# Performance work log

Hardware: AMD Instinct MI355X
Metric: run time of the kernel (lower is better)

The kernel has to match this reference:

```python
import jax, jax.numpy as jnp
import numpy as np

EPS_LN = 1e-6
EPS_NORM = 1e-12


def _l2_normalize(x):
    # F.normalize(p=2, dim=-1): x / max(||x||, eps)
    n = jnp.sqrt(jnp.sum(x * x, axis=-1, keepdims=True))
    return x / jnp.maximum(n, EPS_NORM)


def _layer_norm(x, g, b):
    mu = jnp.mean(x, axis=-1, keepdims=True)
    var = jnp.mean((x - mu) ** 2, axis=-1, keepdims=True)
    return (x - mu) / jnp.sqrt(var + EPS_LN) * g + b


def setup_inputs() -> dict:
    key = jax.random.key(0)
    ks = jax.random.split(key, 4)
    B, S1, S2, H = 16, 2048, 2048, 512
    return {
        "text1_output": jax.random.normal(ks[0], (B, S1, H), dtype=jnp.float32),
        "text2_output": jax.random.normal(ks[1], (B, S2, H), dtype=jnp.float32),
        "text1_mask": jnp.ones((B, S1), dtype=jnp.int32),
        "text2_mask": jnp.ones((B, S2), dtype=jnp.int32),
        "W1": jax.random.normal(ks[2], (H, 2 * H), dtype=jnp.float32) * (1.0 / np.sqrt(H)),
        "b1": jnp.zeros((2 * H,), dtype=jnp.float32),
        "W2": jax.random.normal(ks[3], (2 * H, H), dtype=jnp.float32) * (1.0 / np.sqrt(2 * H)),
        "b2": jnp.zeros((H,), dtype=jnp.float32),
        "ln1_g": jnp.ones((H,), dtype=jnp.float32),
        "ln1_b": jnp.zeros((H,), dtype=jnp.float32),
        "ln2_g": jnp.ones((H,), dtype=jnp.float32),
        "ln2_b": jnp.zeros((H,), dtype=jnp.float32),
    }


def reference(text1_output, text2_output, text1_mask, text2_mask,
              W1, b1, W2, b2, ln1_g, ln1_b, ln2_g, ln2_b):
    # Cosine-similarity cross-attention (dropout = identity, eval mode)
    q_norm = _l2_normalize(text1_output)            # [B,S1,H]
    k_norm = _l2_normalize(text2_output)            # [B,S2,H]
    sim = jnp.einsum('bsh,bth->bst', q_norm, k_norm)  # [B,S1,S2]
    sim = jnp.where(text2_mask[:, None, :] == 0, -jnp.inf, sim)
    attn = jax.nn.softmax(sim, axis=-1)
    out = jnp.einsum('bst,bth->bsh', attn, text2_output)  # [B,S1,H]

    norm_attn = _layer_norm(out, ln1_g, ln1_b)
    resid = norm_attn + text1_output

    ff = jnp.maximum(norm_attn @ W1 + b1, 0.0) @ W2 + b2
    norm_ff = _layer_norm(ff, ln2_g, ln2_b)
    return norm_ff + resid
```

## Files before the change

### kernel.cpp

```cpp
#include <hip/hip_runtime.h>
#include <stdint.h>

#define B_ 16
#define S1_ 2048
#define S2_ 2048
#define H_ 512

typedef short short8 __attribute__((ext_vector_type(8)));
typedef float f32x4 __attribute__((ext_vector_type(4)));

__device__ __forceinline__ unsigned short f2bf(float f) {
  unsigned u = __builtin_bit_cast(unsigned, f);
  u += 0x7fffu + ((u >> 16) & 1u);
  return (unsigned short)(u >> 16);
}
__device__ __forceinline__ float bf2f(unsigned short us) {
  return __builtin_bit_cast(float, (unsigned)us << 16);
}

__device__ __forceinline__ void gload_lds16(const void* g, void* l) {
  __builtin_amdgcn_global_load_lds((const __attribute__((address_space(1))) void*)g,
                                   (__attribute__((address_space(3))) void*)l,
                                   16, 0, 0);
}

__global__ __launch_bounds__(256) void k_cast(const float* __restrict__ x,
                                              unsigned short* __restrict__ y,
                                              float* __restrict__ rn) {
  int row = blockIdx.x * 4 + (threadIdx.x >> 6);
  int l = threadIdx.x & 63;
  const f32x4* xr = (const f32x4*)(x + (size_t)row * H_) + l * 2;
  f32x4 a = xr[0], b = xr[1];
  float s = a[0]*a[0] + a[1]*a[1] + a[2]*a[2] + a[3]*a[3]
          + b[0]*b[0] + b[1]*b[1] + b[2]*b[2] + b[3]*b[3];
#pragma unroll
  for (int m = 1; m < 64; m <<= 1) s += __shfl_xor(s, m);
  if (l == 0) rn[row] = 1.0f / fmaxf(sqrtf(s), 1e-12f);
  short8 o;
#pragma unroll
  for (int i = 0; i < 4; ++i) { o[i] = (short)f2bf(a[i]); o[4 + i] = (short)f2bf(b[i]); }
  *(short8*)(y + (size_t)row * H_ + l * 8) = o;
}

__global__ __launch_bounds__(256) void k_tw(const float* __restrict__ Wm,
                                            unsigned short* __restrict__ WT,
                                            int lgR, int C) {
  int i = blockIdx.x * 256 + threadIdx.x;
  int R = 1 << lgR;
  int n = i >> lgR, k = i & (R - 1);
  WT[i] = f2bf(Wm[(size_t)k * C + n]);
}

__global__ __launch_bounds__(256) void k_tvt(const unsigned short* __restrict__ kn,
                                             unsigned short* __restrict__ vt) {
  __shared__ unsigned short tile[64][72];
  int h0 = blockIdx.x * 64, s0 = blockIdx.y * 64, b = blockIdx.z;
  int t = threadIdx.x;
#pragma unroll
  for (int p = 0; p < 2; ++p) {
    int si = p * 32 + (t >> 3);
    int cj = (t & 7) * 8;
    short8 v = *(const short8*)(kn + ((size_t)(b * S2_ + s0 + si)) * H_ + h0 + cj);
#pragma unroll
    for (int x = 0; x < 8; ++x) tile[si][cj + x] = (unsigned short)v[x];
  }
  __syncthreads();
#pragma unroll
  for (int p = 0; p < 2; ++p) {
    int ho = p * 32 + (t >> 3);
    int sx = (t & 7) * 8;
    short8 o;
#pragma unroll
    for (int x = 0; x < 8; ++x) o[x] = (short)tile[sx + x][ho];
    *(short8*)(vt + ((size_t)(b * H_ + h0 + ho)) * S2_ + s0 + sx) = o;
  }
}

template <int MODE, int SWZ>
__global__ __launch_bounds__(256, 2) void k_gemm(
    const unsigned short* __restrict__ A, const unsigned short* __restrict__ BT,
    const float* __restrict__ bias, const int* __restrict__ mask,
    const float* __restrict__ rq, const float* __restrict__ rk,
    float* __restrict__ lbuf, void* __restrict__ out,
    int M, int N, int K, long sA, long sB, long sOut) {
  __shared__ unsigned short lA[128 * 64];
  __shared__ unsigned short lB[128 * 64];

  int bx, by, z;
  if (SWZ) {
    const int gx = gridDim.x, gy = gridDim.y;
    const int nwg = gx * gy * (int)gridDim.z;
    int orig = ((int)blockIdx.z * gy + (int)blockIdx.y) * gx + (int)blockIdx.x;
    int swzid = ((nwg & 7) == 0) ? ((orig & 7) * (nwg >> 3) + (orig >> 3)) : orig;
    z = swzid / (gx * gy);
    int rem = swzid - z * (gx * gy);
    by = rem / gx;
    bx = rem - by * gx;
  } else {
    bx = blockIdx.x; by = blockIdx.y; z = blockIdx.z;
  }

  const unsigned short* Ab = A + (size_t)z * sA;
  const unsigned short* BTb = BT + (size_t)z * sB;
  const int w = threadIdx.x >> 6, l = threadIdx.x & 63;
  const int lr = l & 15, lk = l >> 4;
  const int m0 = by * 128, n0 = bx * 128;
  const int wm = (w >> 1) * 64, wn = (w & 1) * 64;

  const int srow = l >> 3;
  const int lswz = ((l & 7) * 16) ^ ((srow & 7) << 4);
  const char* pA = (const char*)Ab + ((size_t)(m0 + w * 8 + srow) * K) * 2 + lswz;
  const char* pB = (const char*)BTb + ((size_t)(n0 + w * 8 + srow) * K) * 2 + lswz;
  const size_t rstep = (size_t)K * 64;

  f32x4 acc[4][4];
#pragma unroll
  for (int i = 0; i < 4; ++i)
#pragma unroll
    for (int j = 0; j < 4; ++j) acc[i][j] = (f32x4){0.f, 0.f, 0.f, 0.f};

  const int NT = K >> 6;

#pragma unroll 1
  for (int t = 0; t < NT; ++t) {
    const size_t kb = (size_t)t * 128;
#pragma unroll
    for (int j = 0; j < 4; ++j) {
      gload_lds16(pA + j * rstep + kb, (char*)lA + (j * 4 + w) * 1024);
      gload_lds16(pB + j * rstep + kb, (char*)lB + (j * 4 + w) * 1024);
    }
    asm volatile("s_waitcnt vmcnt(0)" ::: "memory");
    __syncthreads();
#pragma unroll
    for (int s = 0; s < 2; ++s) {
      short8 af[4], bf[4];
#pragma unroll
      for (int mi = 0; mi < 4; ++mi) {
        int row = wm + mi * 16 + lr;
        af[mi] = *(const short8*)(lA + row * 64 + ((s * 32 + lk * 8) ^ ((row & 7) << 3)));
      }
#pragma unroll
      for (int ni = 0; ni < 4; ++ni) {
        int row = wn + ni * 16 + lr;
        bf[ni] = *(const short8*)(lB + row * 64 + ((s * 32 + lk * 8) ^ ((row & 7) << 3)));
      }
#pragma unroll
      for (int mi = 0; mi < 4; ++mi)
#pragma unroll
        for (int ni = 0; ni < 4; ++ni)
          acc[mi][ni] = __builtin_amdgcn_mfma_f32_16x16x32_bf16(af[mi], bf[ni], acc[mi][ni], 0, 0, 0);
    }
    __syncthreads();
  }

  if (MODE == 2) {
    float rqv[4][4], rkv[4], mv[4];
#pragma unroll
    for (int mi = 0; mi < 4; ++mi)
#pragma unroll
      for (int r = 0; r < 4; ++r)
        rqv[mi][r] = rq[(size_t)z * M + m0 + wm + mi * 16 + lk * 4 + r];
#pragma unroll
    for (int ni = 0; ni < 4; ++ni) {
      int gn = n0 + wn + ni * 16 + lr;
      rkv[ni] = rk[(size_t)z * N + gn];
      mv[ni] = (mask[(size_t)z * N + gn] != 0) ? 1.0f : 0.0f;
    }
    float rs[4][4];
#pragma unroll
    for (int mi = 0; mi < 4; ++mi)
#pragma unroll
      for (int r = 0; r < 4; ++r) rs[mi][r] = 0.f;
#pragma unroll
    for (int mi = 0; mi < 4; ++mi)
#pragma unroll
      for (int ni = 0; ni < 4; ++ni) {
        int gn = n0 + wn + ni * 16 + lr;
#pragma unroll
        for (int r = 0; r < 4; ++r) {
          int gm = m0 + wm + mi * 16 + lk * 4 + r;
          float p = __expf(acc[mi][ni][r] * rqv[mi][r] * rkv[ni] - 1.0f) * mv[ni];
          rs[mi][r] += p;
          ((unsigned short*)out)[(size_t)z * sOut + (size_t)gm * N + gn] = f2bf(p);
        }
      }
#pragma unroll
    for (int mi = 0; mi < 4; ++mi)
#pragma unroll
      for (int r = 0; r < 4; ++r) {
        float s = rs[mi][r];
        s += __shfl_xor(s, 1); s += __shfl_xor(s, 2); s += __shfl_xor(s, 4); s += __shfl_xor(s, 8);
        if (lr == 0) {
          int gm = m0 + wm + mi * 16 + lk * 4 + r;
          atomicAdd(&lbuf[(size_t)z * M + gm], s);
        }
      }
  } else if (MODE == 3) {
#pragma unroll
    for (int mi = 0; mi < 4; ++mi)
#pragma unroll
      for (int r = 0; r < 4; ++r) {
        int gm = m0 + wm + mi * 16 + lk * 4 + r;
        float rl = 1.0f / lbuf[(size_t)z * M + gm];
#pragma unroll
        for (int ni = 0; ni < 4; ++ni) {
          int gn = n0 + wn + ni * 16 + lr;
          ((unsigned short*)out)[(size_t)z * sOut + (size_t)gm * N + gn] = f2bf(acc[mi][ni][r] * rl);
        }
      }
  } else {
#pragma unroll
    for (int mi = 0; mi < 4; ++mi)
#pragma unroll
      for (int ni = 0; ni < 4; ++ni) {
        int gn = n0 + wn + ni * 16 + lr;
        float bs = bias[gn];
#pragma unroll
        for (int r = 0; r < 4; ++r) {
          int gm = m0 + wm + mi * 16 + lk * 4 + r;
          float v = acc[mi][ni][r] + bs;
          if (MODE == 0) v = fmaxf(v, 0.f);
          ((unsigned short*)out)[(size_t)gm * N + gn] = f2bf(v);
        }
      }
  }
}

__global__ __launch_bounds__(256) void k_ln1(const unsigned short* __restrict__ O,
                                             const float* __restrict__ g,
                                             const float* __restrict__ bvec,
                                             unsigned short* __restrict__ nattn) {
  int row = blockIdx.x * 4 + (threadIdx.x >> 6);
  int l = threadIdx.x & 63;
  size_t base = (size_t)row * H_ + l * 8;
  short8 ov = *(const short8*)(O + base);
  float x[8];
#pragma unroll
  for (int i = 0; i < 8; ++i) x[i] = bf2f((unsigned short)ov[i]);
  float s = 0.f, q = 0.f;
#pragma unroll
  for (int i = 0; i < 8; ++i) { s += x[i]; q += x[i] * x[i]; }
#pragma unroll
  for (int m = 1; m < 64; m <<= 1) { s += __shfl_xor(s, m); q += __shfl_xor(q, m); }
  float mean = s * (1.f / 512.f);
  float var = q * (1.f / 512.f) - mean * mean;
  float rstd = rsqrtf(var + 1e-6f);
  f32x4 g0 = *(const f32x4*)(g + l * 8), g1v = *(const f32x4*)(g + l * 8 + 4);
  f32x4 b0 = *(const f32x4*)(bvec + l * 8), b1v = *(const f32x4*)(bvec + l * 8 + 4);
  short8 no;
#pragma unroll
  for (int i = 0; i < 4; ++i) {
    no[i]     = (short)f2bf((x[i] - mean) * rstd * g0[i] + b0[i]);
    no[4 + i] = (short)f2bf((x[4 + i] - mean) * rstd * g1v[i] + b1v[i]);
  }
  *(short8*)(nattn + base) = no;
}

__global__ __launch_bounds__(256) void k_ln2(const unsigned short* __restrict__ ff,
                                             const unsigned short* __restrict__ nattn,
                                             const float* __restrict__ text1,
                                             const float* __restrict__ g2,
                                             const float* __restrict__ bb2,
                                             float* __restrict__ out) {
  int row = blockIdx.x * 4 + (threadIdx.x >> 6);
  int l = threadIdx.x & 63;
  size_t base = (size_t)row * H_ + l * 8;
  short8 fv = *(const short8*)(ff + base);
  float x[8];
#pragma unroll
  for (int i = 0; i < 8; ++i) x[i] = bf2f((unsigned short)fv[i]);
  float s = 0.f, q = 0.f;
#pragma unroll
  for (int i = 0; i < 8; ++i) { s += x[i]; q += x[i] * x[i]; }
#pragma unroll
  for (int m = 1; m < 64; m <<= 1) { s += __shfl_xor(s, m); q += __shfl_xor(q, m); }
  float mean = s * (1.f / 512.f);
  float var = q * (1.f / 512.f) - mean * mean;
  float rstd = rsqrtf(var + 1e-6f);
  f32x4 g0 = *(const f32x4*)(g2 + l * 8), g1v = *(const f32x4*)(g2 + l * 8 + 4);
  f32x4 b0 = *(const f32x4*)(bb2 + l * 8), b1v = *(const f32x4*)(bb2 + l * 8 + 4);
  short8 nv = *(const short8*)(nattn + base);
  f32x4 t0 = *(const f32x4*)(text1 + base), t1 = *(const f32x4*)(text1 + base + 4);
  f32x4 o0, o1;
#pragma unroll
  for (int i = 0; i < 4; ++i) {
    o0[i] = (x[i] - mean) * rstd * g0[i] + b0[i] + bf2f((unsigned short)nv[i]) + t0[i];
    o1[i] = (x[4 + i] - mean) * rstd * g1v[i] + b1v[i] + bf2f((unsigned short)nv[4 + i]) + t1[i];
  }
  *(f32x4*)(out + base) = o0;
  *(f32x4*)(out + base + 4) = o1;
}

extern "C" void kernel_launch(void* const* d_in, const int* in_sizes, int n_in,
                              void* d_out, int out_size, void* d_ws, size_t ws_size,
                              hipStream_t stream) {
  const float* text1 = (const float*)d_in[0];
  const float* text2 = (const float*)d_in[1];
  const int* mask2 = (const int*)d_in[3];
  const float* W1 = (const float*)d_in[4];
  const float* b1 = (const float*)d_in[5];
  const float* W2 = (const float*)d_in[6];
  const float* b2 = (const float*)d_in[7];
  const float* g1 = (const float*)d_in[8];
  const float* bb1 = (const float*)d_in[9];
  const float* g2 = (const float*)d_in[10];
  const float* bb2 = (const float*)d_in[11];

  const size_t MiB = 1024ull * 1024ull;
  char* ws = (char*)d_ws;
  unsigned short* W1T   = (unsigned short*)(ws + 0 * MiB);
  unsigned short* W2T   = (unsigned short*)(ws + 1 * MiB);
  float*          lbuf  = (float*)(ws + 2 * MiB);
  float*          rq    = (float*)(ws + 2 * MiB + 256 * 1024);
  float*          rk    = (float*)(ws + 2 * MiB + 512 * 1024);
  unsigned short* qn    = (unsigned short*)(ws + 4 * MiB);
  unsigned short* kn    = (unsigned short*)(ws + 36 * MiB);
  unsigned short* vt    = (unsigned short*)(ws + 68 * MiB);
  unsigned short* P     = (unsigned short*)(ws + 100 * MiB);
  unsigned short* O     = (unsigned short*)(ws + 164 * MiB);
  unsigned short* nattn = (unsigned short*)(ws + 100 * MiB);
  unsigned short* hbuf  = (unsigned short*)(ws + 132 * MiB);
  unsigned short* ffb   = (unsigned short*)(ws + 4 * MiB);
  float* outp = (float*)d_out;

  hipMemsetAsync(lbuf, 0, (size_t)B_ * S1_ * sizeof(float), stream);

  k_cast<<<dim3(B_ * S1_ / 4), 256, 0, stream>>>(text1, qn, rq);
  k_cast<<<dim3(B_ * S2_ / 4), 256, 0, stream>>>(text2, kn, rk);
  k_tw<<<dim3(512 * 1024 / 256), 256, 0, stream>>>(W1, W1T, 9, 1024);
  k_tw<<<dim3(512 * 1024 / 256), 256, 0, stream>>>(W2, W2T, 10, 512);
  k_tvt<<<dim3(H_ / 64, S2_ / 64, B_), 256, 0, stream>>>(kn, vt);

  for (int c = 0; c < 2; ++c) {
    const int c0 = c * 8;
    k_gemm<2, 0><<<dim3(S2_ / 128, S1_ / 128, 8), 256, 0, stream>>>(
        qn + (size_t)c0 * S1_ * H_, kn + (size_t)c0 * S2_ * H_,
        nullptr, mask2 + (size_t)c0 * S2_, rq + (size_t)c0 * S1_, rk + (size_t)c0 * S2_,
        lbuf + (size_t)c0 * S1_, P,
        S1_, S2_, H_, (long)S1_ * H_, (long)S2_ * H_, (long)S1_ * S2_);
    k_gemm<3, 1><<<dim3(H_ / 128, S1_ / 128, 8), 256, 0, stream>>>(
        P, vt + (size_t)c0 * H_ * S2_,
        nullptr, nullptr, nullptr, nullptr,
        lbuf + (size_t)c0 * S1_, O + (size_t)c0 * S1_ * H_,
        S1_, H_, S2_, (long)S1_ * S2_, (long)H_ * S2_, (long)S1_ * H_);
  }

  k_ln1<<<dim3(B_ * S1_ / 4), 256, 0, stream>>>(O, g1, bb1, nattn);
  k_gemm<0, 1><<<dim3(1024 / 128, 32768 / 128, 1), 256, 0, stream>>>(
      nattn, W1T, b1, nullptr, nullptr, nullptr, nullptr, hbuf, 32768, 1024, 512, 0, 0, 0);
  k_gemm<1, 1><<<dim3(512 / 128, 32768 / 128, 1), 256, 0, stream>>>(
      hbuf, W2T, b2, nullptr, nullptr, nullptr, nullptr, ffb, 32768, 512, 1024, 0, 0, 0);
  k_ln2<<<dim3(32768 / 4), 256, 0, stream>>>(ffb, nattn, text1, g2, bb2, outp);
}
```

Baseline: 350.6 us.

## Use FP8 QK similarity GEMM and drop softmax normalization absorbed by LayerNorm

Casts the query and key activations to FP8 e4m3 in the cast kernels and runs the similarity GEMM with FP8 MFMA. Each LDS tile now covers twice the K depth, so global and LDS traffic for that GEMM is halved. It also removes the softmax row-sum accumulation (atomics, memset, and the 1/l scaling in the PV GEMM). This relies on LayerNorm being invariant to a positive per-row scale. The risks are FP8 quantization error in the similarity scores, and a small deviation through the LayerNorm epsilon and bf16 storage of the unnormalized output.

```diff
diff --git a/kernel.cpp b/kernel.cpp
--- a/kernel.cpp
+++ b/kernel.cpp
@@ -24,8 +24,10 @@
                                    16, 0, 0);
 }
 
+template <int WB16>
 __global__ __launch_bounds__(256) void k_cast(const float* __restrict__ x,
                                               unsigned short* __restrict__ y,
+                                              unsigned char* __restrict__ y8,
                                               float* __restrict__ rn) {
   int row = blockIdx.x * 4 + (threadIdx.x >> 6);
   int l = threadIdx.x & 63;
@@ -36,10 +38,18 @@
 #pragma unroll
   for (int m = 1; m < 64; m <<= 1) s += __shfl_xor(s, m);
   if (l == 0) rn[row] = 1.0f / fmaxf(sqrtf(s), 1e-12f);
-  short8 o;
-#pragma unroll
-  for (int i = 0; i < 4; ++i) { o[i] = (short)f2bf(a[i]); o[4 + i] = (short)f2bf(b[i]); }
-  *(short8*)(y + (size_t)row * H_ + l * 8) = o;
+  if (WB16) {
+    short8 o;
+#pragma unroll
+    for (int i = 0; i < 4; ++i) { o[i] = (short)f2bf(a[i]); o[4 + i] = (short)f2bf(b[i]); }
+    *(short8*)(y + (size_t)row * H_ + l * 8) = o;
+  }
+  int p0 = __builtin_amdgcn_cvt_pk_fp8_f32(a[0], a[1], 0, false);
+  p0 = __builtin_amdgcn_cvt_pk_fp8_f32(a[2], a[3], p0, true);
+  int p1 = __builtin_amdgcn_cvt_pk_fp8_f32(b[0], b[1], 0, false);
+  p1 = __builtin_amdgcn_cvt_pk_fp8_f32(b[2], b[3], p1, true);
+  int2 pk = {p0, p1};
+  *(int2*)(y8 + (size_t)row * H_ + l * 8) = pk;
 }
 
 __global__ __launch_bounds__(256) void k_tw(const float* __restrict__ Wm,
@@ -76,15 +86,15 @@
   }
 }
 
-template <int MODE, int SWZ>
+template <int MODE, int SWZ, int FP8>
 __global__ __launch_bounds__(256, 2) void k_gemm(
-    const unsigned short* __restrict__ A, const unsigned short* __restrict__ BT,
+    const void* __restrict__ A, const void* __restrict__ BT,
     const float* __restrict__ bias, const int* __restrict__ mask,
     const float* __restrict__ rq, const float* __restrict__ rk,
-    float* __restrict__ lbuf, void* __restrict__ out,
-    int M, int N, int K, long sA, long sB, long sOut) {
-  __shared__ unsigned short lA[128 * 64];
-  __shared__ unsigned short lB[128 * 64];
+    void* __restrict__ out,
+    int M, int N, int K, long sAbytes, long sBbytes, long sOut) {
+  __shared__ char lA[16384];
+  __shared__ char lB[16384];
 
   int bx, by, z;
   if (SWZ) {
@@ -100,18 +110,17 @@
     bx = blockIdx.x; by = blockIdx.y; z = blockIdx.z;
   }
 
-  const unsigned short* Ab = A + (size_t)z * sA;
-  const unsigned short* BTb = BT + (size_t)z * sB;
   const int w = threadIdx.x >> 6, l = threadIdx.x & 63;
   const int lr = l & 15, lk = l >> 4;
   const int m0 = by * 128, n0 = bx * 128;
   const int wm = (w >> 1) * 64, wn = (w & 1) * 64;
 
+  const size_t rowbytes = (size_t)K * (FP8 ? 1 : 2);
   const int srow = l >> 3;
   const int lswz = ((l & 7) * 16) ^ ((srow & 7) << 4);
-  const char* pA = (const char*)Ab + ((size_t)(m0 + w * 8 + srow) * K) * 2 + lswz;
-  const char* pB = (const char*)BTb + ((size_t)(n0 + w * 8 + srow) * K) * 2 + lswz;
-  const size_t rstep = (size_t)K * 64;
+  const char* pA = (const char*)A + (size_t)z * sAbytes + (size_t)(m0 + w * 8 + srow) * rowbytes + lswz;
+  const char* pB = (const char*)BT + (size_t)z * sBbytes + (size_t)(n0 + w * 8 + srow) * rowbytes + lswz;
+  const size_t rstep = rowbytes * 32;
 
   f32x4 acc[4][4];
 #pragma unroll
@@ -119,36 +128,60 @@
 #pragma unroll
     for (int j = 0; j < 4; ++j) acc[i][j] = (f32x4){0.f, 0.f, 0.f, 0.f};
 
-  const int NT = K >> 6;
+  const int NT = K >> (FP8 ? 7 : 6);
 
 #pragma unroll 1
   for (int t = 0; t < NT; ++t) {
     const size_t kb = (size_t)t * 128;
 #pragma unroll
     for (int j = 0; j < 4; ++j) {
-      gload_lds16(pA + j * rstep + kb, (char*)lA + (j * 4 + w) * 1024);
-      gload_lds16(pB + j * rstep + kb, (char*)lB + (j * 4 + w) * 1024);
+      gload_lds16(pA + j * rstep + kb, lA + (j * 4 + w) * 1024);
+      gload_lds16(pB + j * rstep + kb, lB + (j * 4 + w) * 1024);
     }
     asm volatile("s_waitcnt vmcnt(0)" ::: "memory");
     __syncthreads();
-#pragma unroll
-    for (int s = 0; s < 2; ++s) {
-      short8 af[4], bf[4];
-#pragma unroll
-      for (int mi = 0; mi < 4; ++mi) {
-        int row = wm + mi * 16 + lr;
-        af[mi] = *(const short8*)(lA + row * 64 + ((s * 32 + lk * 8) ^ ((row & 7) << 3)));
-      }
-#pragma unroll
-      for (int ni = 0; ni < 4; ++ni) {
-        int row = wn + ni * 16 + lr;
-        bf[ni] = *(const short8*)(lB + row * 64 + ((s * 32 + lk * 8) ^ ((row & 7) << 3)));
-      }
-#pragma unroll
-      for (int mi = 0; mi < 4; ++mi)
-#pragma unroll
-        for (int ni = 0; ni < 4; ++ni)
-          acc[mi][ni] = __builtin_amdgcn_mfma_f32_16x16x32_bf16(af[mi], bf[ni], acc[mi][ni], 0, 0, 0);
+    if (FP8) {
+#pragma unroll
+      for (int s = 0; s < 4; ++s) {
+        long af[4], bf[4];
+#pragma unroll
+        for (int mi = 0; mi < 4; ++mi) {
+          int row = wm + mi * 16 + lr;
+          af[mi] = *(const long*)(lA + row * 128 + ((s * 32 + lk * 8) ^ ((row & 7) << 4)));
+        }
+#pragma unroll
+        for (int ni = 0; ni < 4; ++ni) {
+          int row = wn + ni * 16 + lr;
+          bf[ni] = *(const long*)(lB + row * 128 + ((s * 32 + lk * 8) ^ ((row & 7) << 4)));
+        }
+#pragma unroll
+        for (int mi = 0; mi < 4; ++mi)
+#pragma unroll
+          for (int ni = 0; ni < 4; ++ni)
+            acc[mi][ni] = __builtin_amdgcn_mfma_f32_16x16x32_fp8_fp8(af[mi], bf[ni], acc[mi][ni], 0, 0, 0);
+      }
+    } else {
+      const unsigned short* As = (const unsigned short*)lA;
+      const unsigned short* Bs = (const unsigned short*)lB;
+#pragma unroll
+      for (int s = 0; s < 2; ++s) {
+        short8 af[4], bf[4];
+#pragma unroll
+        for (int mi = 0; mi < 4; ++mi) {
+          int row = wm + mi * 16 + lr;
+          af[mi] = *(const short8*)(As + row * 64 + ((s * 32 + lk * 8) ^ ((row & 7) << 3)));
+        }
+#pragma unroll
+        for (int ni = 0; ni < 4; ++ni) {
+          int row = wn + ni * 16 + lr;
+          bf[ni] = *(const short8*)(Bs + row * 64 + ((s * 32 + lk * 8) ^ ((row & 7) << 3)));
+        }
+#pragma unroll
+        for (int mi = 0; mi < 4; ++mi)
+#pragma unroll
+          for (int ni = 0; ni < 4; ++ni)
+            acc[mi][ni] = __builtin_amdgcn_mfma_f32_16x16x32_bf16(af[mi], bf[ni], acc[mi][ni], 0, 0, 0);
+      }
     }
     __syncthreads();
   }
@@ -166,11 +199,6 @@
       rkv[ni] = rk[(size_t)z * N + gn];
       mv[ni] = (mask[(size_t)z * N + gn] != 0) ? 1.0f : 0.0f;
     }
-    float rs[4][4];
-#pragma unroll
-    for (int mi = 0; mi < 4; ++mi)
-#pragma unroll
-      for (int r = 0; r < 4; ++r) rs[mi][r] = 0.f;
 #pragma unroll
     for (int mi = 0; mi < 4; ++mi)
 #pragma unroll
@@ -180,19 +208,7 @@
         for (int r = 0; r < 4; ++r) {
           int gm = m0 + wm + mi * 16 + lk * 4 + r;
           float p = __expf(acc[mi][ni][r] * rqv[mi][r] * rkv[ni] - 1.0f) * mv[ni];
-          rs[mi][r] += p;
           ((unsigned short*)out)[(size_t)z * sOut + (size_t)gm * N + gn] = f2bf(p);
-        }
-      }
-#pragma unroll
-    for (int mi = 0; mi < 4; ++mi)
-#pragma unroll
-      for (int r = 0; r < 4; ++r) {
-        float s = rs[mi][r];
-        s += __shfl_xor(s, 1); s += __shfl_xor(s, 2); s += __shfl_xor(s, 4); s += __shfl_xor(s, 8);
-        if (lr == 0) {
-          int gm = m0 + wm + mi * 16 + lk * 4 + r;
-          atomicAdd(&lbuf[(size_t)z * M + gm], s);
         }
       }
   } else if (MODE == 3) {
@@ -201,11 +217,10 @@
 #pragma unroll
       for (int r = 0; r < 4; ++r) {
         int gm = m0 + wm + mi * 16 + lk * 4 + r;
-        float rl = 1.0f / lbuf[(size_t)z * M + gm];
 #pragma unroll
         for (int ni = 0; ni < 4; ++ni) {
           int gn = n0 + wn + ni * 16 + lr;
-          ((unsigned short*)out)[(size_t)z * sOut + (size_t)gm * N + gn] = f2bf(acc[mi][ni][r] * rl);
+          ((unsigned short*)out)[(size_t)z * sOut + (size_t)gm * N + gn] = f2bf(acc[mi][ni][r]);
         }
       }
   } else {
@@ -310,10 +325,10 @@
   char* ws = (char*)d_ws;
   unsigned short* W1T   = (unsigned short*)(ws + 0 * MiB);
   unsigned short* W2T   = (unsigned short*)(ws + 1 * MiB);
-  float*          lbuf  = (float*)(ws + 2 * MiB);
-  float*          rq    = (float*)(ws + 2 * MiB + 256 * 1024);
-  float*          rk    = (float*)(ws + 2 * MiB + 512 * 1024);
-  unsigned short* qn    = (unsigned short*)(ws + 4 * MiB);
+  float*          rq    = (float*)(ws + 2 * MiB);
+  float*          rk    = (float*)(ws + 2 * MiB + 256 * 1024);
+  unsigned char*  qn8   = (unsigned char*)(ws + 4 * MiB);
+  unsigned char*  kn8   = (unsigned char*)(ws + 20 * MiB);
   unsigned short* kn    = (unsigned short*)(ws + 36 * MiB);
   unsigned short* vt    = (unsigned short*)(ws + 68 * MiB);
   unsigned short* P     = (unsigned short*)(ws + 100 * MiB);
@@ -323,32 +338,29 @@
   unsigned short* ffb   = (unsigned short*)(ws + 4 * MiB);
   float* outp = (float*)d_out;
 
-  hipMemsetAsync(lbuf, 0, (size_t)B_ * S1_ * sizeof(float), stream);
-
-  k_cast<<<dim3(B_ * S1_ / 4), 256, 0, stream>>>(text1, qn, rq);
-  k_cast<<<dim3(B_ * S2_ / 4), 256, 0, stream>>>(text2, kn, rk);
+  k_cast<0><<<dim3(B_ * S1_ / 4), 256, 0, stream>>>(text1, nullptr, qn8, rq);
+  k_cast<1><<<dim3(B_ * S2_ / 4), 256, 0, stream>>>(text2, kn, kn8, rk);
   k_tw<<<dim3(512 * 1024 / 256), 256, 0, stream>>>(W1, W1T, 9, 1024);
   k_tw<<<dim3(512 * 1024 / 256), 256, 0, stream>>>(W2, W2T, 10, 512);
   k_tvt<<<dim3(H_ / 64, S2_ / 64, B_), 256, 0, stream>>>(kn, vt);
 
   for (int c = 0; c < 2; ++c) {
     const int c0 = c * 8;
-    k_gemm<2, 0><<<dim3(S2_ / 128, S1_ / 128, 8), 256, 0, stream>>>(
-        qn + (size_t)c0 * S1_ * H_, kn + (size_t)c0 * S2_ * H_,
+    k_gemm<2, 0, 1><<<dim3(S2_ / 128, S1_ / 128, 8), 256, 0, stream>>>(
+        qn8 + (size_t)c0 * S1_ * H_, kn8 + (size_t)c0 * S2_ * H_,
         nullptr, mask2 + (size_t)c0 * S2_, rq + (size_t)c0 * S1_, rk + (size_t)c0 * S2_,
-        lbuf + (size_t)c0 * S1_, P,
-        S1_, S2_, H_, (long)S1_ * H_, (long)S2_ * H_, (long)S1_ * S2_);
-    k_gemm<3, 1><<<dim3(H_ / 128, S1_ / 128, 8), 256, 0, stream>>>(
+        P, S1_, S2_, H_, (long)S1_ * H_, (long)S2_ * H_, (long)S1_ * S2_);
+    k_gemm<3, 1, 0><<<dim3(H_ / 128, S1_ / 128, 8), 256, 0, stream>>>(
         P, vt + (size_t)c0 * H_ * S2_,
         nullptr, nullptr, nullptr, nullptr,
-        lbuf + (size_t)c0 * S1_, O + (size_t)c0 * S1_ * H_,
-        S1_, H_, S2_, (long)S1_ * S2_, (long)H_ * S2_, (long)S1_ * H_);
+        O + (size_t)c0 * S1_ * H_,
+        S1_, H_, S2_, (long)S1_ * S2_ * 2, (long)H_ * S2_ * 2, (long)S1_ * H_);
   }
 
   k_ln1<<<dim3(B_ * S1_ / 4), 256, 0, stream>>>(O, g1, bb1, nattn);
-  k_gemm<0, 1><<<dim3(1024 / 128, 32768 / 128, 1), 256, 0, stream>>>(
-      nattn, W1T, b1, nullptr, nullptr, nullptr, nullptr, hbuf, 32768, 1024, 512, 0, 0, 0);
-  k_gemm<1, 1><<<dim3(512 / 128, 32768 / 128, 1), 256, 0, stream>>>(
-      hbuf, W2T, b2, nullptr, nullptr, nullptr, nullptr, ffb, 32768, 512, 1024, 0, 0, 0);
+  k_gemm<0, 1, 0><<<dim3(1024 / 128, 32768 / 128, 1), 256, 0, stream>>>(
+      nattn, W1T, b1, nullptr, nullptr, nullptr, hbuf, 32768, 1024, 512, 0, 0, 0);
+  k_gemm<1, 1, 0><<<dim3(512 / 128, 32768 / 128, 1), 256, 0, stream>>>(
+      hbuf, W2T, b2, nullptr, nullptr, nullptr, ffb, 32768, 512, 1024, 0, 0, 0);
   k_ln2<<<dim3(32768 / 4), 256, 0, stream>>>(ffb, nattn, text1, g2, bb2, outp);
 }
```

After: 312.7 us. 1.12x faster.
